# Performance work log

Measured on AMD Instinct MI355X. Metric: run time of the kernel, lower is better.

Reference implementation:

```python
import jax, jax.numpy as jnp
import numpy as np

C = 256
R = 4
CR = C // R  # 64


def setup_inputs() -> dict:
    key = jax.random.key(0)
    k1, k2, k3, k4, k5 = jax.random.split(key, 5)
    x = jax.random.normal(k1, (32, C, 112, 112), dtype=jnp.float32)
    # Conv2d kernel_size=1 weights, stored as [out, in] (squeeze the 1x1 spatial dims)
    w1 = jax.random.normal(k2, (CR, C), dtype=jnp.float32) * (1.0 / np.sqrt(C))
    b1 = jax.random.normal(k3, (CR,), dtype=jnp.float32) * 0.01
    w2 = jax.random.normal(k4, (C, CR), dtype=jnp.float32) * (1.0 / np.sqrt(CR))
    b2 = jax.random.normal(k5, (C,), dtype=jnp.float32) * 0.01
    return {"x": x, "w1": w1, "b1": b1, "w2": w2, "b2": b2}


def reference(x, w1, b1, w2, b2):
    # Global average pool over H, W -> [B, C]
    gap = jnp.mean(x, axis=(2, 3))
    # 1x1 conv on a 1x1 map == per-sample matmul
    h = jax.nn.relu(jnp.einsum('bc,oc->bo', gap, w1) + b1)  # [B, C/R]
    attn = jnp.einsum('bo,co->bc', h, w2) + b2              # [B, C]
    gate = jax.nn.sigmoid(attn)[:, :, None, None]            # [B, C, 1, 1]
    return x * gate
```

## Files before the change

### kernel.cpp

```cpp
#include <hip/hip_runtime.h>
#include <math.h>

#define C   256
#define CR  64
#define B   32
#define HW  12544
#define HW4 3136

__global__ __launch_bounds__(256) void gap_kernel(const float* __restrict__ x,
                                                  float* __restrict__ gap) {
    const int bc = blockIdx.x;
    const float4* xp = reinterpret_cast<const float4*>(x) + (size_t)bc * HW4;

    float s = 0.0f;
    for (int i = threadIdx.x; i < HW4; i += 256) {
        float4 v = xp[i];
        s += (v.x + v.y) + (v.z + v.w);
    }
    #pragma unroll
    for (int off = 32; off > 0; off >>= 1)
        s += __shfl_down(s, off, 64);

    __shared__ float wsum[4];
    const int lane = threadIdx.x & 63;
    const int wave = threadIdx.x >> 6;
    if (lane == 0) wsum[wave] = s;
    __syncthreads();
    if (threadIdx.x == 0) {
        float t = (wsum[0] + wsum[1]) + (wsum[2] + wsum[3]);
        gap[bc] = t * (1.0f / (float)HW);
    }
}

__global__ __launch_bounds__(256) void mlp_kernel(const float* __restrict__ gap,
                                                  const float* __restrict__ w1,
                                                  const float* __restrict__ b1,
                                                  const float* __restrict__ w2,
                                                  const float* __restrict__ b2,
                                                  float* __restrict__ gate) {
    const int b = blockIdx.x;
    __shared__ float sg[C];
    __shared__ float sh[CR];

    sg[threadIdx.x] = gap[b * C + threadIdx.x];
    __syncthreads();

    if (threadIdx.x < CR) {
        const int o = threadIdx.x;
        float acc = b1[o];
        const float* wr = w1 + o * C;
        #pragma unroll 8
        for (int c = 0; c < C; ++c) acc = fmaf(sg[c], wr[c], acc);
        sh[o] = fmaxf(acc, 0.0f);
    }
    __syncthreads();

    const int c = threadIdx.x;
    float acc = b2[c];
    const float* wr = w2 + c * CR;
    #pragma unroll 8
    for (int o = 0; o < CR; ++o) acc = fmaf(sh[o], wr[o], acc);
    gate[b * C + c] = 1.0f / (1.0f + expf(-acc));
}

__global__ __launch_bounds__(256) void scale_kernel(const float* __restrict__ x,
                                                    const float* __restrict__ gate,
                                                    float* __restrict__ out) {
    const int bc = blockIdx.x;
    const float g = gate[bc];
    const float4* xp = reinterpret_cast<const float4*>(x)   + (size_t)bc * HW4;
    float4*       op = reinterpret_cast<float4*>(out)       + (size_t)bc * HW4;

    for (int i = threadIdx.x; i < HW4; i += 256) {
        float4 v = xp[i];
        v.x *= g; v.y *= g; v.z *= g; v.w *= g;
        op[i] = v;
    }
}

extern "C" void kernel_launch(void* const* d_in, const int* in_sizes, int n_in,
                              void* d_out, int out_size, void* d_ws, size_t ws_size,
                              hipStream_t stream) {
    const float* x  = (const float*)d_in[0];
    const float* w1 = (const float*)d_in[1];
    const float* b1 = (const float*)d_in[2];
    const float* w2 = (const float*)d_in[3];
    const float* b2 = (const float*)d_in[4];
    float* out = (float*)d_out;

    float* gap  = (float*)d_ws;
    float* gate = gap + B * C;

    gap_kernel<<<B * C, 256, 0, stream>>>(x, gap);
    mlp_kernel<<<B, 256, 0, stream>>>(gap, w1, b1, w2, b2, gate);
    scale_kernel<<<B * C, 256, 0, stream>>>(x, gate, out);
}
```

Baseline: 757.5 us.

## Fuse SE pool, MLP and scale into cooperative persistent kernel processed per batch group

Replaces three separate launches with one cooperative kernel that processes the batch in groups of eight samples, using grid-wide syncs between pooling, the small MLP, and the scaling pass. Grouping keeps each group's slice of x small enough that the second read during scaling may be served from the last-level cache instead of HBM. It adds eight grid barriers and leaves most blocks idle during the tiny MLP phase. It falls back to the original three kernels if the cooperative launch fails.

```diff
diff --git a/kernel.cpp b/kernel.cpp
--- a/kernel.cpp
+++ b/kernel.cpp
@@ -1,17 +1,100 @@
 #include <hip/hip_runtime.h>
+#include <hip/hip_cooperative_groups.h>
 #include <math.h>
 
-#define C   256
-#define CR  64
-#define B   32
-#define HW  12544
-#define HW4 3136
+namespace cg = cooperative_groups;
+
+#define C    256
+#define CR   64
+#define B    32
+#define HW   12544
+#define HW4  3136
+#define BPG  8
+#define NGRP (B / BPG)
+#define PPG  (BPG * C)
+#define NBLK 1024
+#define PPB  (PPG / NBLK)
+
+__global__ __launch_bounds__(256, 4)
+void se_fused(const float* __restrict__ x,
+              const float* __restrict__ w1,
+              const float* __restrict__ b1,
+              const float* __restrict__ w2,
+              const float* __restrict__ b2,
+              float* __restrict__ out,
+              float* __restrict__ gap,
+              float* __restrict__ gate) {
+    cg::grid_group grid = cg::this_grid();
+    __shared__ float sg[C];
+    __shared__ float sh[CR];
+    __shared__ float wsum[4];
+
+    const int tid  = threadIdx.x;
+    const int lane = tid & 63;
+    const int wave = tid >> 6;
+
+    for (int g = 0; g < NGRP; ++g) {
+        const int pbase = g * PPG;
+
+        #pragma unroll
+        for (int p = 0; p < PPB; ++p) {
+            const int plane = pbase + blockIdx.x + p * NBLK;
+            const float4* xp = reinterpret_cast<const float4*>(x) + (size_t)plane * HW4;
+            float s = 0.0f;
+            for (int i = tid; i < HW4; i += 256) {
+                float4 v = xp[i];
+                s += (v.x + v.y) + (v.z + v.w);
+            }
+            #pragma unroll
+            for (int off = 32; off > 0; off >>= 1)
+                s += __shfl_down(s, off, 64);
+            if (lane == 0) wsum[wave] = s;
+            __syncthreads();
+            if (tid == 0)
+                gap[plane] = ((wsum[0] + wsum[1]) + (wsum[2] + wsum[3])) * (1.0f / (float)HW);
+            __syncthreads();
+        }
+        grid.sync();
+
+        if (blockIdx.x < BPG) {
+            const int b = g * BPG + blockIdx.x;
+            sg[tid] = gap[b * C + tid];
+            __syncthreads();
+            if (tid < CR) {
+                float acc = b1[tid];
+                const float* wr = w1 + tid * C;
+                #pragma unroll 8
+                for (int c = 0; c < C; ++c) acc = fmaf(sg[c], wr[c], acc);
+                sh[tid] = fmaxf(acc, 0.0f);
+            }
+            __syncthreads();
+            float acc = b2[tid];
+            const float* wr = w2 + tid * CR;
+            #pragma unroll 8
+            for (int o = 0; o < CR; ++o) acc = fmaf(sh[o], wr[o], acc);
+            gate[b * C + tid] = 1.0f / (1.0f + expf(-acc));
+        }
+        grid.sync();
+
+        #pragma unroll
+        for (int p = 0; p < PPB; ++p) {
+            const int plane = pbase + blockIdx.x + p * NBLK;
+            const float gv = gate[plane];
+            const float4* xp = reinterpret_cast<const float4*>(x) + (size_t)plane * HW4;
+            float4*       op = reinterpret_cast<float4*>(out)     + (size_t)plane * HW4;
+            for (int i = tid; i < HW4; i += 256) {
+                float4 v = xp[i];
+                v.x *= gv; v.y *= gv; v.z *= gv; v.w *= gv;
+                op[i] = v;
+            }
+        }
+    }
+}
 
 __global__ __launch_bounds__(256) void gap_kernel(const float* __restrict__ x,
                                                   float* __restrict__ gap) {
     const int bc = blockIdx.x;
     const float4* xp = reinterpret_cast<const float4*>(x) + (size_t)bc * HW4;
-
     float s = 0.0f;
     for (int i = threadIdx.x; i < HW4; i += 256) {
         float4 v = xp[i];
@@ -20,7 +103,6 @@
     #pragma unroll
     for (int off = 32; off > 0; off >>= 1)
         s += __shfl_down(s, off, 64);
-
     __shared__ float wsum[4];
     const int lane = threadIdx.x & 63;
     const int wave = threadIdx.x >> 6;
@@ -41,10 +123,8 @@
     const int b = blockIdx.x;
     __shared__ float sg[C];
     __shared__ float sh[CR];
-
     sg[threadIdx.x] = gap[b * C + threadIdx.x];
     __syncthreads();
-
     if (threadIdx.x < CR) {
         const int o = threadIdx.x;
         float acc = b1[o];
@@ -54,7 +134,6 @@
         sh[o] = fmaxf(acc, 0.0f);
     }
     __syncthreads();
-
     const int c = threadIdx.x;
     float acc = b2[c];
     const float* wr = w2 + c * CR;
@@ -70,7 +149,6 @@
     const float g = gate[bc];
     const float4* xp = reinterpret_cast<const float4*>(x)   + (size_t)bc * HW4;
     float4*       op = reinterpret_cast<float4*>(out)       + (size_t)bc * HW4;
-
     for (int i = threadIdx.x; i < HW4; i += 256) {
         float4 v = xp[i];
         v.x *= g; v.y *= g; v.z *= g; v.w *= g;
@@ -86,12 +164,18 @@
     const float* b1 = (const float*)d_in[2];
     const float* w2 = (const float*)d_in[3];
     const float* b2 = (const float*)d_in[4];
-    float* out = (float*)d_out;
-
+    float* out  = (float*)d_out;
     float* gap  = (float*)d_ws;
     float* gate = gap + B * C;
 
-    gap_kernel<<<B * C, 256, 0, stream>>>(x, gap);
-    mlp_kernel<<<B, 256, 0, stream>>>(gap, w1, b1, w2, b2, gate);
-    scale_kernel<<<B * C, 256, 0, stream>>>(x, gate, out);
+    void* args[] = { (void*)&x, (void*)&w1, (void*)&b1, (void*)&w2, (void*)&b2,
+                     (void*)&out, (void*)&gap, (void*)&gate };
+    hipError_t err = hipLaunchCooperativeKernel((const void*)se_fused,
+                                                dim3(NBLK), dim3(256),
+                                                args, 0, stream);
+    if (err != hipSuccess) {
+        gap_kernel<<<B * C, 256, 0, stream>>>(x, gap);
+        mlp_kernel<<<B, 256, 0, stream>>>(gap, w1, b1, w2, b2, gate);
+        scale_kernel<<<B * C, 256, 0, stream>>>(x, gate, out);
+    }
 }
```

Measured after the change: 1.641 ms. 2.17x slower.

## Batch plane loads, reverse scale-pass order for cache reuse, use nontemporal stores

Applied to the files above, without the earlier changes.

Both streaming kernels now issue all 12 float4 loads per thread up front, plus a tail load, instead of looping one load at a time. This raises memory-level parallelism. The scale kernel walks planes in reverse order so the planes the GAP pass read last, which may still sit in the large last-level cache, are re-read first. Output writes use nontemporal stores so they do not evict that cached input. The cost is higher register use per thread, and the loop bounds are now hard-coded to the fixed plane size.

```diff
diff --git a/kernel.cpp b/kernel.cpp
--- a/kernel.cpp
+++ b/kernel.cpp
@@ -6,27 +6,37 @@
 #define B   32
 #define HW  12544
 #define HW4 3136
+#define NPLANES (B * C)
+
+typedef float v4f __attribute__((ext_vector_type(4)));
 
 __global__ __launch_bounds__(256) void gap_kernel(const float* __restrict__ x,
                                                   float* __restrict__ gap) {
-    const int bc = blockIdx.x;
-    const float4* xp = reinterpret_cast<const float4*>(x) + (size_t)bc * HW4;
+    const int bc  = blockIdx.x;
+    const int tid = threadIdx.x;
+    const v4f* xp = reinterpret_cast<const v4f*>(x) + (size_t)bc * HW4;
+
+    v4f v[12];
+    #pragma unroll
+    for (int k = 0; k < 12; ++k) v[k] = xp[tid + k * 256];
+    v4f vt;
+    if (tid < 64) vt = xp[3072 + tid];
 
     float s = 0.0f;
-    for (int i = threadIdx.x; i < HW4; i += 256) {
-        float4 v = xp[i];
-        s += (v.x + v.y) + (v.z + v.w);
-    }
+    #pragma unroll
+    for (int k = 0; k < 12; ++k) s += (v[k].x + v[k].y) + (v[k].z + v[k].w);
+    if (tid < 64) s += (vt.x + vt.y) + (vt.z + vt.w);
+
     #pragma unroll
     for (int off = 32; off > 0; off >>= 1)
         s += __shfl_down(s, off, 64);
 
     __shared__ float wsum[4];
-    const int lane = threadIdx.x & 63;
-    const int wave = threadIdx.x >> 6;
+    const int lane = tid & 63;
+    const int wave = tid >> 6;
     if (lane == 0) wsum[wave] = s;
     __syncthreads();
-    if (threadIdx.x == 0) {
+    if (tid == 0) {
         float t = (wsum[0] + wsum[1]) + (wsum[2] + wsum[3]);
         gap[bc] = t * (1.0f / (float)HW);
     }
@@ -66,15 +76,23 @@
 __global__ __launch_bounds__(256) void scale_kernel(const float* __restrict__ x,
                                                     const float* __restrict__ gate,
                                                     float* __restrict__ out) {
-    const int bc = blockIdx.x;
+    const int bc  = (NPLANES - 1) - blockIdx.x;
+    const int tid = threadIdx.x;
     const float g = gate[bc];
-    const float4* xp = reinterpret_cast<const float4*>(x)   + (size_t)bc * HW4;
-    float4*       op = reinterpret_cast<float4*>(out)       + (size_t)bc * HW4;
+    const v4f* xp = reinterpret_cast<const v4f*>(x) + (size_t)bc * HW4;
+    v4f*       op = reinterpret_cast<v4f*>(out)     + (size_t)bc * HW4;
 
-    for (int i = threadIdx.x; i < HW4; i += 256) {
-        float4 v = xp[i];
-        v.x *= g; v.y *= g; v.z *= g; v.w *= g;
-        op[i] = v;
+    v4f v[12];
+    #pragma unroll
+    for (int k = 0; k < 12; ++k) v[k] = xp[tid + k * 256];
+    #pragma unroll
+    for (int k = 0; k < 12; ++k) {
+        v4f r = v[k] * g;
+        __builtin_nontemporal_store(r, op + tid + k * 256);
+    }
+    if (tid < 64) {
+        v4f r = xp[3072 + tid] * g;
+        __builtin_nontemporal_store(r, op + 3072 + tid);
     }
 }
 
@@ -91,7 +109,7 @@
     float* gap  = (float*)d_ws;
     float* gate = gap + B * C;
 
-    gap_kernel<<<B * C, 256, 0, stream>>>(x, gap);
+    gap_kernel<<<NPLANES, 256, 0, stream>>>(x, gap);
     mlp_kernel<<<B, 256, 0, stream>>>(gap, w1, b1, w2, b2, gate);
-    scale_kernel<<<B * C, 256, 0, stream>>>(x, gate, out);
+    scale_kernel<<<NPLANES, 256, 0, stream>>>(x, gate, out);
 }
```

Result: faster. 729.5 us (-3.7%).
